# Kernel tuning notes

Hardware: AMD Instinct MI355X
Metric: run time of the kernel (lower is better)

Reference implementation:

```python
import jax, jax.numpy as jnp
import numpy as np

B, T, N, H, L = 64, 256, 512, 1024, 2


def setup_inputs() -> dict:
    key = jax.random.key(0)
    ks = jax.random.split(key, 12)
    s = 0.02  # weight init scale
    return {
        "x": jax.random.normal(ks[0], (B, T, N), jnp.float32),
        "h": jax.random.normal(ks[1], (L, B, H), jnp.float32),
        "c": jax.random.normal(ks[2], (L, B, H), jnp.float32),
        # layer 0: input dim N
        "W_ih0": jax.random.normal(ks[3], (4 * H, N), jnp.float32) * s,
        "W_hh0": jax.random.normal(ks[4], (4 * H, H), jnp.float32) * s,
        "b_ih0": jax.random.normal(ks[5], (4 * H,), jnp.float32) * s,
        "b_hh0": jax.random.normal(ks[6], (4 * H,), jnp.float32) * s,
        # layer 1: input dim H
        "W_ih1": jax.random.normal(ks[7], (4 * H, H), jnp.float32) * s,
        "W_hh1": jax.random.normal(ks[8], (4 * H, H), jnp.float32) * s,
        "b_ih1": jax.random.normal(ks[9], (4 * H,), jnp.float32) * s,
        "b_hh1": jax.random.normal(ks[10], (4 * H,), jnp.float32) * s,
    }


def _lstm_cell(x_t, h_l, c_l, Wi, Wh, bi, bh):
    # gates: [B, 4H], torch LSTMCell gate order i, f, g, o
    gates = x_t @ Wi.T + h_l @ Wh.T + bi + bh
    i, f, g, o = jnp.split(gates, 4, axis=-1)
    i, f, o = jax.nn.sigmoid(i), jax.nn.sigmoid(f), jax.nn.sigmoid(o)
    g = jnp.tanh(g)
    c_new = f * c_l + i * g
    h_new = o * jnp.tanh(c_new)
    return h_new, c_new


def reference(x, h, c, W_ih0, W_hh0, b_ih0, b_hh0, W_ih1, W_hh1, b_ih1, b_hh1):
    params = [(W_ih0, W_hh0, b_ih0, b_hh0), (W_ih1, W_hh1, b_ih1, b_hh1)]

    def step(carry, x_t):
        h, c = carry  # each [L, B, H]
        inp = x_t
        new_h, new_c = [], []
        for l, (Wi, Wh, bi, bh) in enumerate(params):
            h_new, c_new = _lstm_cell(inp, h[l], c[l], Wi, Wh, bi, bh)
            new_h.append(h_new)
            new_c.append(c_new)
            inp = h_new
        return (jnp.stack(new_h), jnp.stack(new_c)), inp

    xT = jnp.swapaxes(x, 0, 1)  # [T, B, N]
    (h_final, c_final), outsT = jax.lax.scan(step, (h, c), xT)
    outs = jnp.swapaxes(outsT, 0, 1)  # [B, T, H]
    return outs, h_final, c_final
```

## Files before the change

### kernel.cpp

```cpp
#include <hip/hip_runtime.h>
#include <hip/hip_bf16.h>


#define T_ 256
#define B_ 64
#define N_ 512
#define H_ 1024
#define FH_ 4096
#define NWG_SEQ 256
#define BH_ (B_ * H_)

typedef _Float16 f16;
typedef _Float16 f16x4 __attribute__((ext_vector_type(4)));
typedef _Float16 f16x8 __attribute__((ext_vector_type(8)));
typedef float f32x4 __attribute__((ext_vector_type(4)));

template <bool V> struct BC { static constexpr bool value = V; };

__device__ __forceinline__ float sigf(float x) { return 1.f / (1.f + __expf(-x)); }
__device__ __forceinline__ float tanhf_fast(float x) { return 1.f - 2.f / (__expf(2.f * x) + 1.f); }

__device__ __forceinline__ void st_u64g(unsigned long long* p, unsigned long long v) {
  __hip_atomic_store(p, v, __ATOMIC_RELAXED, __HIP_MEMORY_SCOPE_AGENT);
}
__device__ __forceinline__ f16x8 ld_b128_nc(const f16* p) {
  f16x8 r;
  asm volatile("global_load_dwordx4 %0, %1, off sc0 sc1" : "=v"(r) : "v"(p));
  return r;
}

__global__ __launch_bounds__(256) void init_all(
    const float* __restrict__ x, const float* __restrict__ h,
    const float* __restrict__ Wih0, const float* __restrict__ bih0, const float* __restrict__ bhh0,
    const float* __restrict__ Whh0, const float* __restrict__ Wih1, const float* __restrict__ Whh1,
    const float* __restrict__ bih1, const float* __restrict__ bhh1,
    f16* __restrict__ xT, f16* __restrict__ wih0, f16* __restrict__ whh0,
    f16* __restrict__ wih1, f16* __restrict__ whh1,
    float* __restrict__ bias0, float* __restrict__ bias1,
    f16* __restrict__ hinit, unsigned* __restrict__ cnt)
{
  const int stride = gridDim.x * blockDim.x;
  const int t0 = blockIdx.x * blockDim.x + threadIdx.x;

  for (int i = t0; i < T_ * B_ * N_; i += stride) {
    int n = i & (N_ - 1);
    int tb = i >> 9;
    int b = tb & (B_ - 1);
    int t = tb >> 6;
    xT[i] = (f16)x[((size_t)b * T_ + t) * N_ + n];
  }
  for (int i = t0; i < FH_ * N_; i += stride) wih0[i] = (f16)Wih0[i];
  for (int i = t0; i < FH_ * H_; i += stride) {
    whh0[i] = (f16)Whh0[i];
    wih1[i] = (f16)Wih1[i];
    whh1[i] = (f16)Whh1[i];
  }
  for (int i = t0; i < FH_; i += stride) {
    bias0[i] = bih0[i] + bhh0[i];
    bias1[i] = bih1[i] + bhh1[i];
  }
  for (int i = t0; i < 2 * BH_; i += stride) hinit[i] = (f16)h[i];
  if (t0 < 2048) cnt[t0] = 0u;
}

__global__ __launch_bounds__(256) void gemm_pre0(
    const f16* __restrict__ xT, const f16* __restrict__ wih0,
    const float* __restrict__ bias0, f16* __restrict__ pre0T)
{
  const int wid = threadIdx.x >> 6;
  const int lane = threadIdx.x & 63;
  const int lr = lane & 15;
  const int lkq = (lane >> 4) << 3;
  const int lrq = (lane >> 4) << 2;

  const int mt = blockIdx.x & 255;
  const int ct = (blockIdx.x >> 8) * 4 + wid;
  const int row0 = mt * 64, col0 = ct * 64;

  f32x4 acc[4][4] = {};
  const f16* Abase = xT + (size_t)row0 * N_;

  #pragma unroll 2
  for (int kk = 0; kk < N_ / 32; ++kk) {
    const int k = kk * 32 + lkq;
    f16x8 a[4], b[4];
    #pragma unroll
    for (int r = 0; r < 4; ++r)
      a[r] = *(const f16x8*)(Abase + (size_t)(r * 16 + lr) * N_ + k);
    #pragma unroll
    for (int cf = 0; cf < 4; ++cf)
      b[cf] = *(const f16x8*)(wih0 + (size_t)(col0 + cf * 16 + lr) * N_ + k);
    #pragma unroll
    for (int r = 0; r < 4; ++r)
      #pragma unroll
      for (int cf = 0; cf < 4; ++cf)
        acc[r][cf] = __builtin_amdgcn_mfma_f32_16x16x32_f16(a[r], b[cf], acc[r][cf], 0, 0, 0);
  }

  #pragma unroll
  for (int r = 0; r < 4; ++r) {
    #pragma unroll
    for (int cf = 0; cf < 4; ++cf) {
      const int col = col0 + cf * 16 + lr;
      const float bv = bias0[col];
      f16x4 pv;
      #pragma unroll
      for (int ri = 0; ri < 4; ++ri) pv[ri] = (f16)(acc[r][cf][ri] + bv);
      *(f16x4*)(pre0T + ((size_t)mt * FH_ + col) * 64 + r * 16 + lrq) = pv;
    }
  }
}

template <bool DEEP>
__global__ __launch_bounds__(256, 1) void lstm_seq(
    const f16* __restrict__ pre0T, const f16* __restrict__ whh0,
    const f16* __restrict__ wih1, const f16* __restrict__ whh1,
    const float* __restrict__ bias1, const f16* __restrict__ hinit,
    const float* __restrict__ cin,
    f16* __restrict__ h0ring, f16* __restrict__ h1ring,
    f16* __restrict__ h0buf, f16* __restrict__ h1buf,
    float* __restrict__ out, unsigned* __restrict__ cnt)
{
  __shared__ __align__(16) float exc[2][4][32][33];
  __shared__ __align__(16) f16 smH[2][32][8];

  const int tid = threadIdx.x;
  const int p = tid >> 6;
  const int lane = tid & 63;
  const int lr = lane & 15;
  const int lq = lane >> 4;
  const int lkq = lq << 3;
  const int lrq = lq << 2;

  const int wg = blockIdx.x;
  const int pod = wg >> 7;
  const int slot = wg & 127;
  const int rs = pod << 5;
  const int ub = slot << 3;
  unsigned* podc0 = cnt + (size_t)(pod * 2) * 512;
  unsigned* podc1 = cnt + (size_t)(pod * 2 + 1) * 512;

  f16x8 l0w[2][8], l1aw[2][8], l1bw[2][8];
  #pragma unroll
  for (int cf = 0; cf < 2; ++cf) {
    const size_t wr = (size_t)((2 * cf + (lr >> 3)) * H_ + ub + (lr & 7)) * H_;
    #pragma unroll
    for (int j = 0; j < 8; ++j) {
      const int k = (p * 8 + j) * 32 + lkq;
      l0w[cf][j]  = *(const f16x8*)(whh0 + wr + k);
      l1aw[cf][j] = *(const f16x8*)(wih1 + wr + k);
      l1bw[cf][j] = *(const f16x8*)(whh1 + wr + k);
    }
  }

  const int crow = tid & 31;
  const int cu = tid >> 5;
  const size_t cell = (size_t)(rs + crow) * H_ + ub + cu;
  float c0 = cin[cell];
  float c1 = cin[(size_t)BH_ + cell];
  float b1v[4];
  #pragma unroll
  for (int g = 0; g < 4; ++g) b1v[g] = bias1[g * H_ + ub + cu];

  float* outh = out + (size_t)B_ * T_ * H_;
  float* outc = outh + 2 * BH_;

  auto poll = [&](unsigned* word) {
    if (tid == 0) {
      while (__hip_atomic_load(word, __ATOMIC_RELAXED, __HIP_MEMORY_SCOPE_AGENT) < 128u)
        __builtin_amdgcn_s_sleep(1);
    }
    __syncthreads();
  };

  auto body = [&](auto A0c, auto A1c, int e) {
    constexpr bool A0 = decltype(A0c)::value;
    constexpr bool A1 = decltype(A1c)::value;

    float pf[4];
    if (A0) {
      #pragma unroll
      for (int g = 0; g < 4; ++g)
        pf[g] = (float)pre0T[((size_t)e * FH_ + g * H_ + ub + cu) * 64 + rs + crow];
    }

    if (e > 0) poll(&podc0[e - 1]);

    const f16* h0s = ((e == 0) ? hinit
                      : (DEEP ? h0ring + (size_t)(e - 1) * BH_
                              : h0buf + (size_t)((e - 1) & 1) * BH_)) + (size_t)rs * H_;
    f16x8 a0v[8], a1v[8];
    #pragma unroll
    for (int j = 0; j < 8; ++j) {
      const int k = (p * 8 + j) * 32 + lkq;
      if (DEEP) {
        a0v[j] = *(const f16x8*)(h0s + (size_t)lr * H_ + k);
        a1v[j] = *(const f16x8*)(h0s + (size_t)(16 + lr) * H_ + k);
      } else {
        a0v[j] = ld_b128_nc(h0s + (size_t)lr * H_ + k);
        a1v[j] = ld_b128_nc(h0s + (size_t)(16 + lr) * H_ + k);
      }
    }
    if (!DEEP) {
      asm volatile("s_waitcnt vmcnt(0)" ::: "memory");
      __builtin_amdgcn_sched_barrier(0);
    }

    f32x4 acc0[2][2] = {};
    f32x4 acc1[2][2] = {};
    #pragma unroll
    for (int j = 0; j < 8; ++j) {
      if (A0) {
        #pragma unroll
        for (int cf = 0; cf < 2; ++cf) {
          acc0[cf][0] = __builtin_amdgcn_mfma_f32_16x16x32_f16(a0v[j], l0w[cf][j], acc0[cf][0], 0, 0, 0);
          acc0[cf][1] = __builtin_amdgcn_mfma_f32_16x16x32_f16(a1v[j], l0w[cf][j], acc0[cf][1], 0, 0, 0);
        }
      }
      if (A1) {
        #pragma unroll
        for (int cf = 0; cf < 2; ++cf) {
          acc1[cf][0] = __builtin_amdgcn_mfma_f32_16x16x32_f16(a0v[j], l1aw[cf][j], acc1[cf][0], 0, 0, 0);
          acc1[cf][1] = __builtin_amdgcn_mfma_f32_16x16x32_f16(a1v[j], l1aw[cf][j], acc1[cf][1], 0, 0, 0);
        }
      }
    }

    if (A0) {
      #pragma unroll
      for (int cf = 0; cf < 2; ++cf)
        #pragma unroll
        for (int rf = 0; rf < 2; ++rf)
          #pragma unroll
          for (int ri = 0; ri < 4; ++ri)
            exc[0][p][rf * 16 + lrq + ri][cf * 16 + lr] = acc0[cf][rf][ri];
      __syncthreads();

      float gv[4];
      #pragma unroll
      for (int g = 0; g < 4; ++g)
        gv[g] = exc[0][0][crow][g * 8 + cu] + exc[0][1][crow][g * 8 + cu]
              + exc[0][2][crow][g * 8 + cu] + exc[0][3][crow][g * 8 + cu] + pf[g];
      const float cn = sigf(gv[1]) * c0 + sigf(gv[0]) * tanhf_fast(gv[2]);
      const float hn = sigf(gv[3]) * tanhf_fast(cn);
      c0 = cn;
      smH[0][crow][cu] = (f16)hn;
      if (e == T_ - 1) { outh[cell] = hn; outc[cell] = cn; }
      __syncthreads();

      if (p == 0) {
        const int row = lane >> 1, half = lane & 1;
        unsigned long long v = *(const unsigned long long*)&smH[0][row][half * 4];
        f16* dst = DEEP ? h0ring + (size_t)e * BH_ : h0buf + (size_t)(e & 1) * BH_;
        st_u64g((unsigned long long*)(dst + (size_t)(rs + row) * H_ + ub + half * 4), v);
      }
      asm volatile("s_waitcnt vmcnt(0)" ::: "memory");
      if (tid == 0)
        (void)__hip_atomic_fetch_add(&podc0[e], 1u, __ATOMIC_RELAXED, __HIP_MEMORY_SCOPE_AGENT);
    }

    if (A1) {
      if (e >= 2) poll(&podc1[e - 1]);

      const f16* h1s = ((e == 1) ? hinit + BH_
                        : (DEEP ? h1ring + (size_t)(e - 2) * BH_
                                : h1buf + (size_t)(e & 1) * BH_)) + (size_t)rs * H_;
      f16x8 c0v[8], c1v[8];
      #pragma unroll
      for (int j = 0; j < 8; ++j) {
        const int k = (p * 8 + j) * 32 + lkq;
        if (DEEP) {
          c0v[j] = *(const f16x8*)(h1s + (size_t)lr * H_ + k);
          c1v[j] = *(const f16x8*)(h1s + (size_t)(16 + lr) * H_ + k);
        } else {
          c0v[j] = ld_b128_nc(h1s + (size_t)lr * H_ + k);
          c1v[j] = ld_b128_nc(h1s + (size_t)(16 + lr) * H_ + k);
        }
      }
      if (!DEEP) {
        asm volatile("s_waitcnt vmcnt(0)" ::: "memory");
        __builtin_amdgcn_sched_barrier(0);
      }

      #pragma unroll
      for (int j = 0; j < 8; ++j) {
        #pragma unroll
        for (int cf = 0; cf < 2; ++cf) {
          acc1[cf][0] = __builtin_amdgcn_mfma_f32_16x16x32_f16(c0v[j], l1bw[cf][j], acc1[cf][0], 0, 0, 0);
          acc1[cf][1] = __builtin_amdgcn_mfma_f32_16x16x32_f16(c1v[j], l1bw[cf][j], acc1[cf][1], 0, 0, 0);
        }
      }

      #pragma unroll
      for (int cf = 0; cf < 2; ++cf)
        #pragma unroll
        for (int rf = 0; rf < 2; ++rf)
          #pragma unroll
          for (int ri = 0; ri < 4; ++ri)
            exc[1][p][rf * 16 + lrq + ri][cf * 16 + lr] = acc1[cf][rf][ri];
      __syncthreads();

      const int t = e - 1;
      float gv[4];
      #pragma unroll
      for (int g = 0; g < 4; ++g)
        gv[g] = exc[1][0][crow][g * 8 + cu] + exc[1][1][crow][g * 8 + cu]
              + exc[1][2][crow][g * 8 + cu] + exc[1][3][crow][g * 8 + cu] + b1v[g];
      const float cn = sigf(gv[1]) * c1 + sigf(gv[0]) * tanhf_fast(gv[2]);
      const float hn = sigf(gv[3]) * tanhf_fast(cn);
      c1 = cn;
      smH[1][crow][cu] = (f16)hn;
      out[(size_t)(rs + crow) * (T_ * H_) + (size_t)t * H_ + ub + cu] = hn;
      if (e == T_) { outh[BH_ + cell] = hn; outc[BH_ + cell] = cn; }
      __syncthreads();

      if (p == 1) {
        const int row = lane >> 1, half = lane & 1;
        unsigned long long v = *(const unsigned long long*)&smH[1][row][half * 4];
        f16* dst = DEEP ? h1ring + (size_t)(e - 1) * BH_ : h1buf + (size_t)((e - 1) & 1) * BH_;
        st_u64g((unsigned long long*)(dst + (size_t)(rs + row) * H_ + ub + half * 4), v);
      }
      asm volatile("s_waitcnt vmcnt(0)" ::: "memory");
      if (tid == 64)
        (void)__hip_atomic_fetch_add(&podc1[e], 1u, __ATOMIC_RELAXED, __HIP_MEMORY_SCOPE_AGENT);
    }
  };

  body(BC<true>{}, BC<false>{}, 0);
  for (int e = 1; e < T_; ++e) body(BC<true>{}, BC<true>{}, e);
  body(BC<false>{}, BC<true>{}, T_);
}

extern "C" void kernel_launch(void* const* d_in, const int* in_sizes, int n_in,
                              void* d_out, int out_size, void* d_ws, size_t ws_size,
                              hipStream_t stream)
{
  const float* x    = (const float*)d_in[0];
  const float* h    = (const float*)d_in[1];
  const float* c    = (const float*)d_in[2];
  const float* Wih0 = (const float*)d_in[3];
  const float* Whh0 = (const float*)d_in[4];
  const float* bih0 = (const float*)d_in[5];
  const float* bhh0 = (const float*)d_in[6];
  const float* Wih1 = (const float*)d_in[7];
  const float* Whh1 = (const float*)d_in[8];
  const float* bih1 = (const float*)d_in[9];
  const float* bhh1 = (const float*)d_in[10];

  char* w = (char*)d_ws;
  size_t off = 0;
  auto carve = [&](size_t bytes) -> char* {
    char* ptr = w + off;
    off = (off + bytes + 255) & ~(size_t)255;
    return ptr;
  };
  f16*   pre0T = (f16*)  carve((size_t)T_ * B_ * FH_ * 2);
  f16*   xT    = (f16*)  carve((size_t)T_ * B_ * N_ * 2);
  f16*   wih0  = (f16*)  carve((size_t)FH_ * N_ * 2);
  f16*   whh0  = (f16*)  carve((size_t)FH_ * H_ * 2);
  f16*   wih1  = (f16*)  carve((size_t)FH_ * H_ * 2);
  f16*   whh1  = (f16*)  carve((size_t)FH_ * H_ * 2);
  float* bias0 = (float*)carve((size_t)FH_ * 4);
  float* bias1 = (float*)carve((size_t)FH_ * 4);
  f16*   hinit = (f16*)  carve((size_t)2 * BH_ * 2);
  f16*   h0buf = (f16*)  carve((size_t)2 * BH_ * 2);
  f16*   h1buf = (f16*)  carve((size_t)2 * BH_ * 2);
  unsigned* cnt = (unsigned*)carve(2048 * 4);
  const size_t base_end = off;
  f16*   h0ring = (f16*) carve((size_t)T_ * BH_ * 2);
  f16*   h1ring = (f16*) carve((size_t)T_ * BH_ * 2);
  const bool deep = (off <= ws_size);
  if (base_end > ws_size) return;

  init_all<<<2048, 256, 0, stream>>>(x, h, Wih0, bih0, bhh0, Whh0, Wih1, Whh1, bih1, bhh1,
                                     xT, wih0, whh0, wih1, whh1, bias0, bias1, hinit, cnt);
  gemm_pre0<<<4096, 256, 0, stream>>>(xT, wih0, bias0, pre0T);
  if (deep)
    lstm_seq<true><<<NWG_SEQ, 256, 0, stream>>>(pre0T, whh0, wih1, whh1, bias1, hinit,
                                                (const float*)c, h0ring, h1ring, h0buf, h1buf,
                                                (float*)d_out, cnt);
  else
    lstm_seq<false><<<NWG_SEQ, 256, 0, stream>>>(pre0T, whh0, wih1, whh1, bias1, hinit,
                                                 (const float*)c, h0ring, h1ring, h0buf, h1buf,
                                                 (float*)d_out, cnt);
}
```

Measured before the change: 1.934 ms.

## Split persistent LSTM workgroups into dedicated layer-0 and layer-1 roles

Before, every workgroup computed both layers for one timestep offset, running a layer-0 and a layer-1 phase in each step. Now half the workgroups in each pod own layer 0 and the other half own layer 1, each covering 16 hidden units with all four gates. The two layers run as a pipeline synchronised through per-step counters, and the non-deep path uses an 8-deep ring with back-pressure polling. The aim is to shorten the serial critical path of each step by letting layer 1 lag layer 0. The cost is more register-resident weights per workgroup (4x8 fragments, or two such sets for layer 1) and extra barriers.

```diff
diff --git a/kernel.cpp b/kernel.cpp
--- a/kernel.cpp
+++ b/kernel.cpp
@@ -14,19 +14,23 @@
 typedef _Float16 f16x4 __attribute__((ext_vector_type(4)));
 typedef _Float16 f16x8 __attribute__((ext_vector_type(8)));
 typedef float f32x4 __attribute__((ext_vector_type(4)));
-
-template <bool V> struct BC { static constexpr bool value = V; };
+typedef unsigned long long ull;
 
 __device__ __forceinline__ float sigf(float x) { return 1.f / (1.f + __expf(-x)); }
 __device__ __forceinline__ float tanhf_fast(float x) { return 1.f - 2.f / (__expf(2.f * x) + 1.f); }
 
-__device__ __forceinline__ void st_u64g(unsigned long long* p, unsigned long long v) {
+__device__ __forceinline__ void st_u64g(ull* p, ull v) {
   __hip_atomic_store(p, v, __ATOMIC_RELAXED, __HIP_MEMORY_SCOPE_AGENT);
 }
 __device__ __forceinline__ f16x8 ld_b128_nc(const f16* p) {
   f16x8 r;
   asm volatile("global_load_dwordx4 %0, %1, off sc0 sc1" : "=v"(r) : "v"(p));
   return r;
+}
+template <bool CACHED>
+__device__ __forceinline__ f16x8 ldf(const f16* p) {
+  if constexpr (CACHED) return *(const f16x8*)p;
+  else return ld_b128_nc(p);
 }
 
 __global__ __launch_bounds__(256) void init_all(
@@ -117,12 +121,11 @@
     const f16* __restrict__ wih1, const f16* __restrict__ whh1,
     const float* __restrict__ bias1, const f16* __restrict__ hinit,
     const float* __restrict__ cin,
-    f16* __restrict__ h0ring, f16* __restrict__ h1ring,
-    f16* __restrict__ h0buf, f16* __restrict__ h1buf,
+    f16* __restrict__ h0r, f16* __restrict__ h1r,
     float* __restrict__ out, unsigned* __restrict__ cnt)
 {
-  __shared__ __align__(16) float exc[2][4][32][33];
-  __shared__ __align__(16) f16 smH[2][32][8];
+  __shared__ __align__(16) float exc[4][4][32][17];
+  __shared__ __align__(16) f16 smH[32][16];
 
   const int tid = threadIdx.x;
   const int p = tid >> 6;
@@ -135,200 +138,214 @@
   const int wg = blockIdx.x;
   const int pod = wg >> 7;
   const int slot = wg & 127;
+  const int role = slot >> 6;
+  const int us = (slot & 63) << 4;
   const int rs = pod << 5;
-  const int ub = slot << 3;
-  unsigned* podc0 = cnt + (size_t)(pod * 2) * 512;
-  unsigned* podc1 = cnt + (size_t)(pod * 2 + 1) * 512;
-
-  f16x8 l0w[2][8], l1aw[2][8], l1bw[2][8];
-  #pragma unroll
-  for (int cf = 0; cf < 2; ++cf) {
-    const size_t wr = (size_t)((2 * cf + (lr >> 3)) * H_ + ub + (lr & 7)) * H_;
-    #pragma unroll
-    for (int j = 0; j < 8; ++j) {
-      const int k = (p * 8 + j) * 32 + lkq;
-      l0w[cf][j]  = *(const f16x8*)(whh0 + wr + k);
-      l1aw[cf][j] = *(const f16x8*)(wih1 + wr + k);
-      l1bw[cf][j] = *(const f16x8*)(whh1 + wr + k);
-    }
-  }
-
-  const int crow = tid & 31;
-  const int cu = tid >> 5;
-  const size_t cell = (size_t)(rs + crow) * H_ + ub + cu;
-  float c0 = cin[cell];
-  float c1 = cin[(size_t)BH_ + cell];
-  float b1v[4];
-  #pragma unroll
-  for (int g = 0; g < 4; ++g) b1v[g] = bias1[g * H_ + ub + cu];
+
+  unsigned* cnt0 = cnt + pod * 512;
+  unsigned* cnt1 = cnt + 1024 + pod * 512;
+
+  const int rc0 = tid >> 4;
+  const int uc = tid & 15;
+  const int rc1 = rc0 + 16;
+  const size_t cellA = (size_t)(rs + rc0) * H_ + us + uc;
+  const size_t cellB = (size_t)(rs + rc1) * H_ + us + uc;
 
   float* outh = out + (size_t)B_ * T_ * H_;
   float* outc = outh + 2 * BH_;
 
-  auto poll = [&](unsigned* word) {
+  auto rt = [&](int t) -> size_t { return DEEP ? (size_t)t : (size_t)(t & 7); };
+  auto pollw = [&](unsigned* w2) {
     if (tid == 0) {
-      while (__hip_atomic_load(word, __ATOMIC_RELAXED, __HIP_MEMORY_SCOPE_AGENT) < 128u)
+      while (__hip_atomic_load(w2, __ATOMIC_RELAXED, __HIP_MEMORY_SCOPE_AGENT) < 64u)
         __builtin_amdgcn_s_sleep(1);
     }
-    __syncthreads();
   };
 
-  auto body = [&](auto A0c, auto A1c, int e) {
-    constexpr bool A0 = decltype(A0c)::value;
-    constexpr bool A1 = decltype(A1c)::value;
-
-    float pf[4];
-    if (A0) {
-      #pragma unroll
-      for (int g = 0; g < 4; ++g)
-        pf[g] = (float)pre0T[((size_t)e * FH_ + g * H_ + ub + cu) * 64 + rs + crow];
-    }
-
-    if (e > 0) poll(&podc0[e - 1]);
-
-    const f16* h0s = ((e == 0) ? hinit
-                      : (DEEP ? h0ring + (size_t)(e - 1) * BH_
-                              : h0buf + (size_t)((e - 1) & 1) * BH_)) + (size_t)rs * H_;
-    f16x8 a0v[8], a1v[8];
-    #pragma unroll
-    for (int j = 0; j < 8; ++j) {
-      const int k = (p * 8 + j) * 32 + lkq;
-      if (DEEP) {
-        a0v[j] = *(const f16x8*)(h0s + (size_t)lr * H_ + k);
-        a1v[j] = *(const f16x8*)(h0s + (size_t)(16 + lr) * H_ + k);
-      } else {
-        a0v[j] = ld_b128_nc(h0s + (size_t)lr * H_ + k);
-        a1v[j] = ld_b128_nc(h0s + (size_t)(16 + lr) * H_ + k);
-      }
-    }
-    if (!DEEP) {
-      asm volatile("s_waitcnt vmcnt(0)" ::: "memory");
-      __builtin_amdgcn_sched_barrier(0);
-    }
-
-    f32x4 acc0[2][2] = {};
-    f32x4 acc1[2][2] = {};
-    #pragma unroll
-    for (int j = 0; j < 8; ++j) {
-      if (A0) {
+  if (role == 0) {
+    f16x8 w0[4][8];
+    #pragma unroll
+    for (int cf = 0; cf < 4; ++cf)
+      #pragma unroll
+      for (int j = 0; j < 8; ++j)
+        w0[cf][j] = *(const f16x8*)(whh0 + (size_t)(cf * H_ + us + lr) * H_ + (p * 8 + j) * 32 + lkq);
+
+    float cA = cin[cellA], cB = cin[cellB];
+
+    for (int e = 0; e < T_; ++e) {
+      float pfA[4], pfB[4];
+      #pragma unroll
+      for (int g = 0; g < 4; ++g) {
+        pfA[g] = (float)pre0T[((size_t)e * FH_ + g * H_ + us + uc) * 64 + rs + rc0];
+        pfB[g] = (float)pre0T[((size_t)e * FH_ + g * H_ + us + uc) * 64 + rs + rc1];
+      }
+
+      if (e > 0) pollw(&cnt0[e - 1]);
+      if (!DEEP && e >= 8) pollw(&cnt1[e - 8]);
+      __syncthreads();
+
+      const f16* src = ((e == 0) ? hinit : h0r + rt(e - 1) * BH_) + (size_t)rs * H_;
+      f16x8 af0[8], af1[8];
+      #pragma unroll
+      for (int j = 0; j < 8; ++j) {
+        const int k = (p * 8 + j) * 32 + lkq;
+        af0[j] = ldf<DEEP>(src + (size_t)lr * H_ + k);
+        af1[j] = ldf<DEEP>(src + (size_t)(16 + lr) * H_ + k);
+      }
+      if (!DEEP) {
+        asm volatile("s_waitcnt vmcnt(0)" ::: "memory");
+        __builtin_amdgcn_sched_barrier(0);
+      }
+
+      f32x4 acc[4][2] = {};
+      #pragma unroll
+      for (int j = 0; j < 8; ++j)
         #pragma unroll
-        for (int cf = 0; cf < 2; ++cf) {
-          acc0[cf][0] = __builtin_amdgcn_mfma_f32_16x16x32_f16(a0v[j], l0w[cf][j], acc0[cf][0], 0, 0, 0);
-          acc0[cf][1] = __builtin_amdgcn_mfma_f32_16x16x32_f16(a1v[j], l0w[cf][j], acc0[cf][1], 0, 0, 0);
+        for (int cf = 0; cf < 4; ++cf) {
+          acc[cf][0] = __builtin_amdgcn_mfma_f32_16x16x32_f16(af0[j], w0[cf][j], acc[cf][0], 0, 0, 0);
+          acc[cf][1] = __builtin_amdgcn_mfma_f32_16x16x32_f16(af1[j], w0[cf][j], acc[cf][1], 0, 0, 0);
         }
-      }
-      if (A1) {
-        #pragma unroll
-        for (int cf = 0; cf < 2; ++cf) {
-          acc1[cf][0] = __builtin_amdgcn_mfma_f32_16x16x32_f16(a0v[j], l1aw[cf][j], acc1[cf][0], 0, 0, 0);
-          acc1[cf][1] = __builtin_amdgcn_mfma_f32_16x16x32_f16(a1v[j], l1aw[cf][j], acc1[cf][1], 0, 0, 0);
-        }
-      }
-    }
-
-    if (A0) {
-      #pragma unroll
-      for (int cf = 0; cf < 2; ++cf)
+
+      #pragma unroll
+      for (int cf = 0; cf < 4; ++cf)
         #pragma unroll
         for (int rf = 0; rf < 2; ++rf)
           #pragma unroll
           for (int ri = 0; ri < 4; ++ri)
-            exc[0][p][rf * 16 + lrq + ri][cf * 16 + lr] = acc0[cf][rf][ri];
-      __syncthreads();
-
-      float gv[4];
-      #pragma unroll
-      for (int g = 0; g < 4; ++g)
-        gv[g] = exc[0][0][crow][g * 8 + cu] + exc[0][1][crow][g * 8 + cu]
-              + exc[0][2][crow][g * 8 + cu] + exc[0][3][crow][g * 8 + cu] + pf[g];
-      const float cn = sigf(gv[1]) * c0 + sigf(gv[0]) * tanhf_fast(gv[2]);
-      const float hn = sigf(gv[3]) * tanhf_fast(cn);
-      c0 = cn;
-      smH[0][crow][cu] = (f16)hn;
-      if (e == T_ - 1) { outh[cell] = hn; outc[cell] = cn; }
+            exc[p][cf][rf * 16 + lrq + ri][lr] = acc[cf][rf][ri];
+      __syncthreads();
+
+      float gvA[4], gvB[4];
+      #pragma unroll
+      for (int g = 0; g < 4; ++g) {
+        gvA[g] = exc[0][g][rc0][uc] + exc[1][g][rc0][uc]
+               + exc[2][g][rc0][uc] + exc[3][g][rc0][uc] + pfA[g];
+        gvB[g] = exc[0][g][rc1][uc] + exc[1][g][rc1][uc]
+               + exc[2][g][rc1][uc] + exc[3][g][rc1][uc] + pfB[g];
+      }
+      const float cnA = sigf(gvA[1]) * cA + sigf(gvA[0]) * tanhf_fast(gvA[2]);
+      const float hnA = sigf(gvA[3]) * tanhf_fast(cnA);
+      const float cnB = sigf(gvB[1]) * cB + sigf(gvB[0]) * tanhf_fast(gvB[2]);
+      const float hnB = sigf(gvB[3]) * tanhf_fast(cnB);
+      cA = cnA; cB = cnB;
+      smH[rc0][uc] = (f16)hnA;
+      smH[rc1][uc] = (f16)hnB;
       __syncthreads();
 
       if (p == 0) {
-        const int row = lane >> 1, half = lane & 1;
-        unsigned long long v = *(const unsigned long long*)&smH[0][row][half * 4];
-        f16* dst = DEEP ? h0ring + (size_t)e * BH_ : h0buf + (size_t)(e & 1) * BH_;
-        st_u64g((unsigned long long*)(dst + (size_t)(rs + row) * H_ + ub + half * 4), v);
+        const int row = lane >> 1, u8 = (lane & 1) * 8;
+        f16* dst = h0r + rt(e) * BH_ + (size_t)(rs + row) * H_ + us + u8;
+        st_u64g((ull*)dst, *(const ull*)&smH[row][u8]);
+        st_u64g((ull*)(dst + 4), *(const ull*)&smH[row][u8 + 4]);
       }
       asm volatile("s_waitcnt vmcnt(0)" ::: "memory");
+      __syncthreads();
       if (tid == 0)
-        (void)__hip_atomic_fetch_add(&podc0[e], 1u, __ATOMIC_RELAXED, __HIP_MEMORY_SCOPE_AGENT);
+        (void)__hip_atomic_fetch_add(&cnt0[e], 1u, __ATOMIC_RELAXED, __HIP_MEMORY_SCOPE_AGENT);
+
+      if (e == T_ - 1) {
+        outh[cellA] = hnA; outc[cellA] = cnA;
+        outh[cellB] = hnB; outc[cellB] = cnB;
+      }
     }
-
-    if (A1) {
-      if (e >= 2) poll(&podc1[e - 1]);
-
-      const f16* h1s = ((e == 1) ? hinit + BH_
-                        : (DEEP ? h1ring + (size_t)(e - 2) * BH_
-                                : h1buf + (size_t)(e & 1) * BH_)) + (size_t)rs * H_;
-      f16x8 c0v[8], c1v[8];
+  } else {
+    f16x8 wa[4][8], wb[4][8];
+    #pragma unroll
+    for (int cf = 0; cf < 4; ++cf)
+      #pragma unroll
+      for (int j = 0; j < 8; ++j) {
+        const size_t wr = (size_t)(cf * H_ + us + lr) * H_ + (p * 8 + j) * 32 + lkq;
+        wa[cf][j] = *(const f16x8*)(wih1 + wr);
+        wb[cf][j] = *(const f16x8*)(whh1 + wr);
+      }
+
+    float cA = cin[BH_ + cellA], cB = cin[BH_ + cellB];
+    float b1[4];
+    #pragma unroll
+    for (int g = 0; g < 4; ++g) b1[g] = bias1[g * H_ + us + uc];
+
+    for (int e = 0; e < T_; ++e) {
+      pollw(&cnt0[e]);
+      if (e > 0) pollw(&cnt1[e - 1]);
+      __syncthreads();
+
+      const f16* s0 = h0r + rt(e) * BH_ + (size_t)rs * H_;
+      const f16* s1 = ((e == 0) ? hinit + BH_ : h1r + rt(e - 1) * BH_) + (size_t)rs * H_;
+      f16x8 a0[8], a1[8], d0[8], d1[8];
       #pragma unroll
       for (int j = 0; j < 8; ++j) {
         const int k = (p * 8 + j) * 32 + lkq;
-        if (DEEP) {
-          c0v[j] = *(const f16x8*)(h1s + (size_t)lr * H_ + k);
-          c1v[j] = *(const f16x8*)(h1s + (size_t)(16 + lr) * H_ + k);
-        } else {
-          c0v[j] = ld_b128_nc(h1s + (size_t)lr * H_ + k);
-          c1v[j] = ld_b128_nc(h1s + (size_t)(16 + lr) * H_ + k);
-        }
+        a0[j] = ldf<DEEP>(s0 + (size_t)lr * H_ + k);
+        a1[j] = ldf<DEEP>(s0 + (size_t)(16 + lr) * H_ + k);
+        d0[j] = ldf<DEEP>(s1 + (size_t)lr * H_ + k);
+        d1[j] = ldf<DEEP>(s1 + (size_t)(16 + lr) * H_ + k);
       }
       if (!DEEP) {
         asm volatile("s_waitcnt vmcnt(0)" ::: "memory");
         __builtin_amdgcn_sched_barrier(0);
       }
 
-      #pragma unroll
-      for (int j = 0; j < 8; ++j) {
+      f32x4 acc[4][2] = {};
+      #pragma unroll
+      for (int j = 0; j < 8; ++j)
         #pragma unroll
-        for (int cf = 0; cf < 2; ++cf) {
-          acc1[cf][0] = __builtin_amdgcn_mfma_f32_16x16x32_f16(c0v[j], l1bw[cf][j], acc1[cf][0], 0, 0, 0);
-          acc1[cf][1] = __builtin_amdgcn_mfma_f32_16x16x32_f16(c1v[j], l1bw[cf][j], acc1[cf][1], 0, 0, 0);
+        for (int cf = 0; cf < 4; ++cf) {
+          acc[cf][0] = __builtin_amdgcn_mfma_f32_16x16x32_f16(a0[j], wa[cf][j], acc[cf][0], 0, 0, 0);
+          acc[cf][1] = __builtin_amdgcn_mfma_f32_16x16x32_f16(a1[j], wa[cf][j], acc[cf][1], 0, 0, 0);
         }
-      }
-
-      #pragma unroll
-      for (int cf = 0; cf < 2; ++cf)
+      #pragma unroll
+      for (int j = 0; j < 8; ++j)
+        #pragma unroll
+        for (int cf = 0; cf < 4; ++cf) {
+          acc[cf][0] = __builtin_amdgcn_mfma_f32_16x16x32_f16(d0[j], wb[cf][j], acc[cf][0], 0, 0, 0);
+          acc[cf][1] = __builtin_amdgcn_mfma_f32_16x16x32_f16(d1[j], wb[cf][j], acc[cf][1], 0, 0, 0);
+        }
+
+      #pragma unroll
+      for (int cf = 0; cf < 4; ++cf)
         #pragma unroll
         for (int rf = 0; rf < 2; ++rf)
           #pragma unroll
           for (int ri = 0; ri < 4; ++ri)
-            exc[1][p][rf * 16 + lrq + ri][cf * 16 + lr] = acc1[cf][rf][ri];
-      __syncthreads();
-
-      const int t = e - 1;
-      float gv[4];
-      #pragma unroll
-      for (int g = 0; g < 4; ++g)
-        gv[g] = exc[1][0][crow][g * 8 + cu] + exc[1][1][crow][g * 8 + cu]
-              + exc[1][2][crow][g * 8 + cu] + exc[1][3][crow][g * 8 + cu] + b1v[g];
-      const float cn = sigf(gv[1]) * c1 + sigf(gv[0]) * tanhf_fast(gv[2]);
-      const float hn = sigf(gv[3]) * tanhf_fast(cn);
-      c1 = cn;
-      smH[1][crow][cu] = (f16)hn;
-      out[(size_t)(rs + crow) * (T_ * H_) + (size_t)t * H_ + ub + cu] = hn;
-      if (e == T_) { outh[BH_ + cell] = hn; outc[BH_ + cell] = cn; }
-      __syncthreads();
-
-      if (p == 1) {
-        const int row = lane >> 1, half = lane & 1;
-        unsigned long long v = *(const unsigned long long*)&smH[1][row][half * 4];
-        f16* dst = DEEP ? h1ring + (size_t)(e - 1) * BH_ : h1buf + (size_t)((e - 1) & 1) * BH_;
-        st_u64g((unsigned long long*)(dst + (size_t)(rs + row) * H_ + ub + half * 4), v);
+            exc[p][cf][rf * 16 + lrq + ri][lr] = acc[cf][rf][ri];
+      __syncthreads();
+
+      float gvA[4], gvB[4];
+      #pragma unroll
+      for (int g = 0; g < 4; ++g) {
+        gvA[g] = exc[0][g][rc0][uc] + exc[1][g][rc0][uc]
+               + exc[2][g][rc0][uc] + exc[3][g][rc0][uc] + b1[g];
+        gvB[g] = exc[0][g][rc1][uc] + exc[1][g][rc1][uc]
+               + exc[2][g][rc1][uc] + exc[3][g][rc1][uc] + b1[g];
+      }
+      const float cnA = sigf(gvA[1]) * cA + sigf(gvA[0]) * tanhf_fast(gvA[2]);
+      const float hnA = sigf(gvA[3]) * tanhf_fast(cnA);
+      const float cnB = sigf(gvB[1]) * cB + sigf(gvB[0]) * tanhf_fast(gvB[2]);
+      const float hnB = sigf(gvB[3]) * tanhf_fast(cnB);
+      cA = cnA; cB = cnB;
+      smH[rc0][uc] = (f16)hnA;
+      smH[rc1][uc] = (f16)hnB;
+      __syncthreads();
+
+      if (p == 0) {
+        const int row = lane >> 1, u8 = (lane & 1) * 8;
+        f16* dst = h1r + rt(e) * BH_ + (size_t)(rs + row) * H_ + us + u8;
+        st_u64g((ull*)dst, *(const ull*)&smH[row][u8]);
+        st_u64g((ull*)(dst + 4), *(const ull*)&smH[row][u8 + 4]);
       }
       asm volatile("s_waitcnt vmcnt(0)" ::: "memory");
-      if (tid == 64)
-        (void)__hip_atomic_fetch_add(&podc1[e], 1u, __ATOMIC_RELAXED, __HIP_MEMORY_SCOPE_AGENT);
+      __syncthreads();
+      if (tid == 0)
+        (void)__hip_atomic_fetch_add(&cnt1[e], 1u, __ATOMIC_RELAXED, __HIP_MEMORY_SCOPE_AGENT);
+
+      out[(size_t)(rs + rc0) * (T_ * H_) + (size_t)e * H_ + us + uc] = hnA;
+      out[(size_t)(rs + rc1) * (T_ * H_) + (size_t)e * H_ + us + uc] = hnB;
+      if (e == T_ - 1) {
+        outh[BH_ + cellA] = hnA; outc[BH_ + cellA] = cnA;
+        outh[BH_ + cellB] = hnB; outc[BH_ + cellB] = cnB;
+      }
     }
-  };
-
-  body(BC<true>{}, BC<false>{}, 0);
-  for (int e = 1; e < T_; ++e) body(BC<true>{}, BC<true>{}, e);
-  body(BC<false>{}, BC<true>{}, T_);
+  }
 }
 
 extern "C" void kernel_launch(void* const* d_in, const int* in_sizes, int n_in,
@@ -363,8 +380,8 @@
   float* bias0 = (float*)carve((size_t)FH_ * 4);
   float* bias1 = (float*)carve((size_t)FH_ * 4);
   f16*   hinit = (f16*)  carve((size_t)2 * BH_ * 2);
-  f16*   h0buf = (f16*)  carve((size_t)2 * BH_ * 2);
-  f16*   h1buf = (f16*)  carve((size_t)2 * BH_ * 2);
+  f16*   h0s   = (f16*)  carve((size_t)8 * BH_ * 2);
+  f16*   h1s   = (f16*)  carve((size_t)8 * BH_ * 2);
   unsigned* cnt = (unsigned*)carve(2048 * 4);
   const size_t base_end = off;
   f16*   h0ring = (f16*) carve((size_t)T_ * BH_ * 2);
@@ -377,10 +394,10 @@
   gemm_pre0<<<4096, 256, 0, stream>>>(xT, wih0, bias0, pre0T);
   if (deep)
     lstm_seq<true><<<NWG_SEQ, 256, 0, stream>>>(pre0T, whh0, wih1, whh1, bias1, hinit,
-                                                (const float*)c, h0ring, h1ring, h0buf, h1buf,
+                                                (const float*)c, h0ring, h1ring,
                                                 (float*)d_out, cnt);
   else
     lstm_seq<false><<<NWG_SEQ, 256, 0, stream>>>(pre0T, whh0, wih1, whh1, bias1, hinit,
-                                                 (const float*)c, h0ring, h1ring, h0buf, h1buf,
+                                                 (const float*)c, h0s, h1s,
                                                  (float*)d_out, cnt);
 }
```

After: 2.956 ms. +52.8%, slower.
